# Performance work log

Measured on AMD Instinct MI355X. Metric: run time of the kernel, lower is better.

## Reference

```python
import jax, jax.numpy as jnp
import numpy as np

B, S, D_MODEL, D_INT = 4, 2048, 1024, 512
ALPHA = 0.3


def setup_inputs() -> dict:
    key = jax.random.key(0)
    ks = jax.random.split(key, 8)
    scale = 1.0 / np.sqrt(D_MODEL)
    inp = {
        "z_real": jax.random.normal(ks[0], (B, S, D_MODEL), dtype=jnp.float32),
        "z_imag": jax.random.normal(ks[1], (B, S, D_MODEL), dtype=jnp.float32),
        "Wq_r": jax.random.normal(ks[2], (D_MODEL, D_INT), dtype=jnp.float32) * scale,
        "Wq_i": jax.random.normal(ks[3], (D_MODEL, D_INT), dtype=jnp.float32) * scale,
        "Wk_r": jax.random.normal(ks[4], (D_MODEL, D_INT), dtype=jnp.float32) * scale,
        "Wk_i": jax.random.normal(ks[5], (D_MODEL, D_INT), dtype=jnp.float32) * scale,
        "Wv_r": jax.random.normal(ks[6], (D_MODEL, D_INT), dtype=jnp.float32) * scale,
        "Wv_i": jax.random.normal(ks[7], (D_MODEL, D_INT), dtype=jnp.float32) * scale,
    }
    return inp


def _complex_proj(zr, zi, Wr, Wi):
    # (zr + i*zi) @ (Wr + i*Wi) computed via 4 real matmuls, as in the torch code
    out_r = zr @ Wr - zi @ Wi
    out_i = zi @ Wr + zr @ Wi
    return out_r + 1j * out_i  # complex64


def reference(z_real, z_imag, Wq_r, Wq_i, Wk_r, Wk_i, Wv_r, Wv_i):
    q = _complex_proj(z_real, z_imag, Wq_r, Wq_i)  # [B,S,D_INT] complex64
    k = _complex_proj(z_real, z_imag, Wk_r, Wk_i)
    v = _complex_proj(z_real, z_imag, Wv_r, Wv_i)

    # attn_scores = q @ k^H : [B,S,S] complex64
    attn_scores = jnp.einsum("bsd,btd->bst", q, jnp.conj(k))

    # variant == 'hybrid': (|scores| + alpha*cos(angle(scores))) / sqrt(d_k)
    mag = jnp.abs(attn_scores)
    phase = jnp.cos(jnp.angle(attn_scores))
    scores = (mag + ALPHA * phase) / np.sqrt(D_INT)

    attn_weights = jax.nn.softmax(scores, axis=-1)  # [B,S,S] float32
    output = jnp.einsum("bst,btd->bsd", attn_weights.astype(jnp.complex64), v)
    return output, attn_weights
```

## Files before the change

### kernel.cpp

```cpp
#include <hip/hip_runtime.h>
#include <hip/hip_bf16.h>

typedef unsigned short u16;
typedef u16   u16x4 __attribute__((ext_vector_type(4)));
typedef u16   u16x8 __attribute__((ext_vector_type(8)));
typedef short v8s   __attribute__((ext_vector_type(8)));
typedef float fx4   __attribute__((ext_vector_type(4)));

#define DEVINL __device__ __forceinline__

DEVINL u16 f2bf(float x){
    unsigned u = __float_as_uint(x);
    u = u + 0x7FFFu + ((u >> 16) & 1u);
    return (u16)(u >> 16);
}
DEVINL float bf2f(u16 h){ return __uint_as_float(((unsigned)h) << 16); }

DEVINL void gload16(const u16* g, u16* l){
    __builtin_amdgcn_global_load_lds(
        (const __attribute__((address_space(1))) void*)g,
        (__attribute__((address_space(3))) void*)l, 16, 0, 0);
}

__global__ void convZ_kernel(const float* __restrict__ zr, const float* __restrict__ zi,
                             u16* __restrict__ Zh, u16* __restrict__ Zl){
    int idx = blockIdx.x * blockDim.x + threadIdx.x;
    size_t i4 = (size_t)idx * 4;
    int m = (int)(i4 >> 11);
    int c = (int)(i4 & 2047);
    const float* src = (c < 1024) ? (zr + (size_t)m*1024 + c)
                                  : (zi + (size_t)m*1024 + (c - 1024));
    fx4 v = *(const fx4*)src;
    u16x4 h, l;
#pragma unroll
    for (int j = 0; j < 4; j++){
        u16 hh = f2bf(v[j]); h[j] = hh; l[j] = f2bf(v[j] - bf2f(hh));
    }
    *(u16x4*)(Zh + i4) = h;
    *(u16x4*)(Zl + i4) = l;
}

__global__ void convW_kernel(const float* __restrict__ Wq_r, const float* __restrict__ Wq_i,
                             const float* __restrict__ Wk_r, const float* __restrict__ Wk_i,
                             const float* __restrict__ Wv_r, const float* __restrict__ Wv_i,
                             u16* __restrict__ Wth, u16* __restrict__ Wtl){
    __shared__ float t[32][33];
    int k0 = blockIdx.x * 32;
    int c0 = blockIdx.y * 32;
    int blk = c0 >> 9;  int j0 = c0 & 511;
    int pair = blk >> 1, ri = blk & 1;
    int hh = k0 >> 10;  int ks0 = k0 & 1023;
    const float* Ws[6] = {Wq_r, Wq_i, Wk_r, Wk_i, Wv_r, Wv_i};
    const float* src; float sign = 1.f;
    if (ri == 0){ if (hh == 0) src = Ws[pair*2]; else { src = Ws[pair*2+1]; sign = -1.f; } }
    else        { src = (hh == 0) ? Ws[pair*2+1] : Ws[pair*2]; }
    int tx = threadIdx.x, ty = threadIdx.y;
    for (int yy = ty; yy < 32; yy += 8)
        t[yy][tx] = src[(size_t)(ks0 + yy)*512 + j0 + tx];
    __syncthreads();
    for (int yy = ty; yy < 32; yy += 8){
        float v = sign * t[tx][yy];
        u16 h2 = f2bf(v);
        size_t o = (size_t)(c0 + yy)*2048 + k0 + tx;
        Wth[o] = h2;
        Wtl[o] = f2bf(v - bf2f(h2));
    }
}

__global__ void vt_kernel(const u16* __restrict__ C, int colOff, u16* __restrict__ Vt){
    __shared__ u16 t[32][34];
    int t0 = blockIdx.x * 32; int d0 = blockIdx.y * 32; int b = blockIdx.z;
    int tx = threadIdx.x, ty = threadIdx.y;
    const u16* src = C + (size_t)b*2048*3072 + colOff;
    for (int yy = ty; yy < 32; yy += 8)
        t[yy][tx] = src[(size_t)(t0 + yy)*3072 + d0 + tx];
    __syncthreads();
    u16* dst = Vt + (size_t)b*512*2048;
    for (int yy = ty; yy < 32; yy += 8)
        dst[(size_t)(d0 + yy)*2048 + t0 + tx] = t[tx][yy];
}

__global__ __launch_bounds__(256)
void softmax_kernel(float* __restrict__ H, const float* __restrict__ SiP, u16* __restrict__ Wbf){
    int row = blockIdx.x;
    float* p = H + (size_t)row * 2048;
    const float* q = SiP + (size_t)row * 2048;
    int tid = threadIdx.x;
    fx4 v[2];
#pragma unroll
    for (int i = 0; i < 2; i++){
        fx4 sr = *(fx4*)(p + i*1024 + tid*4);
        fx4 si = *(const fx4*)(q + i*1024 + tid*4);
#pragma unroll
        for (int j = 0; j < 4; j++){
            float mag = sqrtf(sr[j]*sr[j] + si[j]*si[j]);
            float ph  = sr[j] / fmaxf(mag, 1e-30f);
            v[i][j] = (mag + 0.3f*ph) * 0.044194173824159216f;
        }
    }
    float m = -1e30f;
#pragma unroll
    for (int i = 0; i < 2; i++)
#pragma unroll
        for (int j = 0; j < 4; j++) m = fmaxf(m, v[i][j]);
    for (int k = 1; k < 64; k <<= 1) m = fmaxf(m, __shfl_xor(m, k));
    __shared__ float sm[4], ss[4];
    int w = tid >> 6, lane = tid & 63;
    if (lane == 0) sm[w] = m;
    __syncthreads();
    m = fmaxf(fmaxf(sm[0], sm[1]), fmaxf(sm[2], sm[3]));
    float s = 0.f;
#pragma unroll
    for (int i = 0; i < 2; i++)
#pragma unroll
        for (int j = 0; j < 4; j++){ v[i][j] = __expf(v[i][j] - m); s += v[i][j]; }
    for (int k = 1; k < 64; k <<= 1) s += __shfl_xor(s, k);
    if (lane == 0) ss[w] = s;
    __syncthreads();
    s = ss[0] + ss[1] + ss[2] + ss[3];
    float inv = 1.f / s;
    u16* wb = Wbf + (size_t)row * 2048;
#pragma unroll
    for (int i = 0; i < 2; i++){
        fx4 o; u16x4 ob;
#pragma unroll
        for (int j = 0; j < 4; j++){ o[j] = v[i][j] * inv; ob[j] = f2bf(o[j]); }
        *(fx4*)(p + i*1024 + tid*4) = o;
        *(u16x4*)(wb + i*1024 + tid*4) = ob;
    }
}

__global__ __launch_bounds__(256, 2)
void score2_kernel(const u16* __restrict__ Chi, const u16* __restrict__ Clo,
                   float* __restrict__ Sr, float* __restrict__ Si)
{
    __shared__ u16 smem[8 * 4096];
    int z = blockIdx.z;
    int tid = threadIdx.x, lane = tid & 63, w = tid >> 6;
    int wm = w & 1, wn = w >> 1;
    int frow = lane & 15, g = lane >> 4;

    int srow = w * 32 + (lane >> 2);
    int scol = (lane & 3) * 8;
    size_t qoff = ((size_t)z*2048 + blockIdx.y*128 + srow) * 3072 + scol;
    size_t koff = ((size_t)z*2048 + blockIdx.x*128 + srow) * 3072 + 1024 + scol;
    u16* L = smem;

    v8s sgn8;
#pragma unroll
    for (int j = 0; j < 8; j++) sgn8[j] = (short)0x8000;

    fx4 aR[4][4] = {}, aI[4][4] = {};

    for (int kt = 0; kt < 16; ++kt){
        int k0 = kt * 32;
#pragma unroll
        for (int c = 0; c < 2; c++){
            size_t q = qoff + (size_t)c * 49152 + k0;
            size_t k = koff + (size_t)c * 49152 + k0;
            u16* d = L + w * 1024 + c * 512;
            gload16(Chi + q,       d);
            gload16(Clo + q,       d + 4096);
            gload16(Chi + q + 512, d + 8192);
            gload16(Clo + q + 512, d + 12288);
            gload16(Chi + k,       d + 16384);
            gload16(Clo + k,       d + 20480);
            gload16(Chi + k + 512, d + 24576);
            gload16(Clo + k + 512, d + 28672);
        }
        __syncthreads();

        v8s ar_h[4], ar_l[4], ai_h[4], ai_l[4];
#pragma unroll
        for (int mi = 0; mi < 4; mi++){
            int off = (wm*64 + mi*16 + frow) * 32 + g * 8;
            ar_h[mi] = *(const v8s*)(L + off);
            ar_l[mi] = *(const v8s*)(L + 4096  + off);
            ai_h[mi] = *(const v8s*)(L + 8192  + off);
            ai_l[mi] = *(const v8s*)(L + 12288 + off);
        }
#pragma unroll
        for (int ni = 0; ni < 4; ni++){
            int off = (wn*64 + ni*16 + frow) * 32 + g * 8;
            v8s br_h = *(const v8s*)(L + 16384 + off);
            v8s br_l = *(const v8s*)(L + 20480 + off);
            v8s bi_h = *(const v8s*)(L + 24576 + off);
            v8s bi_l = *(const v8s*)(L + 28672 + off);
            v8s bn_h = bi_h ^ sgn8;
            v8s bn_l = bi_l ^ sgn8;
#pragma unroll
            for (int mi = 0; mi < 4; mi++){
                aR[mi][ni] = __builtin_amdgcn_mfma_f32_16x16x32_bf16(ar_h[mi], br_h, aR[mi][ni], 0, 0, 0);
                aR[mi][ni] = __builtin_amdgcn_mfma_f32_16x16x32_bf16(ar_h[mi], br_l, aR[mi][ni], 0, 0, 0);
                aR[mi][ni] = __builtin_amdgcn_mfma_f32_16x16x32_bf16(ar_l[mi], br_h, aR[mi][ni], 0, 0, 0);
                aR[mi][ni] = __builtin_amdgcn_mfma_f32_16x16x32_bf16(ai_h[mi], bi_h, aR[mi][ni], 0, 0, 0);
                aR[mi][ni] = __builtin_amdgcn_mfma_f32_16x16x32_bf16(ai_h[mi], bi_l, aR[mi][ni], 0, 0, 0);
                aR[mi][ni] = __builtin_amdgcn_mfma_f32_16x16x32_bf16(ai_l[mi], bi_h, aR[mi][ni], 0, 0, 0);
                aI[mi][ni] = __builtin_amdgcn_mfma_f32_16x16x32_bf16(ai_h[mi], br_h, aI[mi][ni], 0, 0, 0);
                aI[mi][ni] = __builtin_amdgcn_mfma_f32_16x16x32_bf16(ai_h[mi], br_l, aI[mi][ni], 0, 0, 0);
                aI[mi][ni] = __builtin_amdgcn_mfma_f32_16x16x32_bf16(ai_l[mi], br_h, aI[mi][ni], 0, 0, 0);
                aI[mi][ni] = __builtin_amdgcn_mfma_f32_16x16x32_bf16(ar_h[mi], bn_h, aI[mi][ni], 0, 0, 0);
                aI[mi][ni] = __builtin_amdgcn_mfma_f32_16x16x32_bf16(ar_h[mi], bn_l, aI[mi][ni], 0, 0, 0);
                aI[mi][ni] = __builtin_amdgcn_mfma_f32_16x16x32_bf16(ar_l[mi], bn_h, aI[mi][ni], 0, 0, 0);
            }
        }
        __syncthreads();
    }

    size_t cb = (size_t)z * 2048 * 2048;
    int gcol0 = blockIdx.x * 128 + wn * 64;
    int grow0 = blockIdx.y * 128 + wm * 64;
    int rgrp  = (lane >> 4) * 4;
#pragma unroll
    for (int mi = 0; mi < 4; mi++)
#pragma unroll
        for (int ni = 0; ni < 4; ni++){
            int col = gcol0 + ni*16 + frow;
#pragma unroll
            for (int r = 0; r < 4; r++){
                size_t o = cb + (size_t)(grow0 + mi*16 + rgrp + r) * 2048 + col;
                Sr[o] = aR[mi][ni][r];
                Si[o] = aI[mi][ni][r];
            }
        }
}

template<int SPLIT, int EPI>
__global__ __launch_bounds__(256, 2)
void gemm_bt(const u16* __restrict__ Ah, const u16* __restrict__ Al,
             long long aBatch, int lda,
             const u16* __restrict__ Bh, const u16* __restrict__ Bl,
             long long bBatch, int ldb,
             float* __restrict__ Cf, u16* __restrict__ Ch, u16* __restrict__ Cl,
             long long cBatch, int ldc, int ostride, int nk)
{
    constexpr int NT = SPLIT ? 4 : 2;
    __shared__ u16 smem[NT * 8192];

    int z = blockIdx.z;
    const u16* Ab  = Ah + (size_t)(aBatch * z) + (size_t)blockIdx.y * 128 * lda;
    const u16* Bb  = Bh + (size_t)(bBatch * z) + (size_t)blockIdx.x * 128 * ldb;

    int tid = threadIdx.x;
    int lane = tid & 63, w = tid >> 6;
    int wm = w & 1, wn = w >> 1;
    int frow = lane & 15, g = lane >> 4;

    int srow = w * 32 + (lane >> 3);
    int slog = (lane & 7) ^ (lane >> 3);
    const u16* pA  = Ab + (size_t)srow * lda + slog * 8;
    const u16* pB  = Bb + (size_t)srow * ldb + slog * 8;
    const u16* pAl = nullptr; const u16* pBl = nullptr;
    if constexpr (SPLIT){
        pAl = Al + (size_t)(aBatch * z) + (size_t)blockIdx.y * 128 * lda + (size_t)srow * lda + slog * 8;
        pBl = Bl + (size_t)(bBatch * z) + (size_t)blockIdx.x * 128 * ldb + (size_t)srow * ldb + slog * 8;
    }
    u16* ldsA  = smem + w * 2048;
    u16* ldsB  = smem + 8192 + w * 2048;
    u16* ldsAl = smem + 16384 + w * 2048;
    u16* ldsBl = smem + 24576 + w * 2048;

    fx4 acc[4][4] = {};

    for (int kt = 0; kt < nk; ++kt){
#pragma unroll
        for (int c = 0; c < 4; c++){
            size_t ga = (size_t)c * 8 * lda;
            size_t gb = (size_t)c * 8 * ldb;
            gload16(pA + ga, ldsA + c * 512);
            gload16(pB + gb, ldsB + c * 512);
            if constexpr (SPLIT){
                gload16(pAl + ga, ldsAl + c * 512);
                gload16(pBl + gb, ldsBl + c * 512);
            }
        }
        __syncthreads();

#pragma unroll
        for (int s = 0; s < 2; s++){
            int ko = ((g + 4*s) ^ (frow & 7)) * 8;
            v8s a_h[4], b_h[4];
#pragma unroll
            for (int mi = 0; mi < 4; mi++)
                a_h[mi] = *(const v8s*)(smem + (wm*64 + mi*16 + frow)*64 + ko);
#pragma unroll
            for (int ni = 0; ni < 4; ni++)
                b_h[ni] = *(const v8s*)(smem + 8192 + (wn*64 + ni*16 + frow)*64 + ko);
            if constexpr (SPLIT){
                v8s a_l[4], b_l[4];
#pragma unroll
                for (int mi = 0; mi < 4; mi++)
                    a_l[mi] = *(const v8s*)(smem + 16384 + (wm*64 + mi*16 + frow)*64 + ko);
#pragma unroll
                for (int ni = 0; ni < 4; ni++)
                    b_l[ni] = *(const v8s*)(smem + 24576 + (wn*64 + ni*16 + frow)*64 + ko);
#pragma unroll
                for (int mi = 0; mi < 4; mi++)
#pragma unroll
                    for (int ni = 0; ni < 4; ni++){
                        acc[mi][ni] = __builtin_amdgcn_mfma_f32_16x16x32_bf16(a_h[mi], b_h[ni], acc[mi][ni], 0, 0, 0);
                        acc[mi][ni] = __builtin_amdgcn_mfma_f32_16x16x32_bf16(a_h[mi], b_l[ni], acc[mi][ni], 0, 0, 0);
                        acc[mi][ni] = __builtin_amdgcn_mfma_f32_16x16x32_bf16(a_l[mi], b_h[ni], acc[mi][ni], 0, 0, 0);
                    }
            } else {
#pragma unroll
                for (int mi = 0; mi < 4; mi++)
#pragma unroll
                    for (int ni = 0; ni < 4; ni++)
                        acc[mi][ni] = __builtin_amdgcn_mfma_f32_16x16x32_bf16(a_h[mi], b_h[ni], acc[mi][ni], 0, 0, 0);
            }
        }
        __syncthreads();
        pA += 64; pB += 64;
        if constexpr (SPLIT){ pAl += 64; pBl += 64; }
    }

    int gcol0 = blockIdx.x * 128 + wn * 64;
    int grow0 = blockIdx.y * 128 + wm * 64;
    int rgrp  = (lane >> 4) * 4;
    if constexpr (EPI == 0){
        float* Cb = Cf + (size_t)(cBatch * z);
#pragma unroll
        for (int mi = 0; mi < 4; mi++)
#pragma unroll
            for (int ni = 0; ni < 4; ni++){
                int col = gcol0 + ni*16 + frow;
#pragma unroll
                for (int r = 0; r < 4; r++){
                    int row = grow0 + mi*16 + rgrp + r;
                    Cb[((size_t)row * ldc + col) * (size_t)ostride] = acc[mi][ni][r];
                }
            }
    } else {
        u16* Chb = Ch + (size_t)(cBatch * z);
        u16* Clb = Cl + (size_t)(cBatch * z);
#pragma unroll
        for (int mi = 0; mi < 4; mi++)
#pragma unroll
            for (int ni = 0; ni < 4; ni++){
                int col = gcol0 + ni*16 + frow;
#pragma unroll
                for (int r = 0; r < 4; r++){
                    int row = grow0 + mi*16 + rgrp + r;
                    float v = acc[mi][ni][r];
                    u16 hh = f2bf(v);
                    size_t o = (size_t)row * ldc + col;
                    Chb[o] = hh;
                    Clb[o] = f2bf(v - bf2f(hh));
                }
            }
    }
}

extern "C" void kernel_launch(void* const* d_in, const int* in_sizes, int n_in,
                              void* d_out, int out_size, void* d_ws, size_t ws_size,
                              hipStream_t stream)
{
    const float* zr   = (const float*)d_in[0];
    const float* zi   = (const float*)d_in[1];
    const float* Wq_r = (const float*)d_in[2];
    const float* Wq_i = (const float*)d_in[3];
    const float* Wk_r = (const float*)d_in[4];
    const float* Wk_i = (const float*)d_in[5];
    const float* Wv_r = (const float*)d_in[6];
    const float* Wv_i = (const float*)d_in[7];

    constexpr long long Bn = 4, S = 2048, DI = 512;
    char* ws = (char*)d_ws;
    u16* Chi = (u16*)ws;
    u16* Clo = Chi + 25165824;
    char* ws2 = ws + 134217728;
    u16* Zh  = (u16*)ws2;
    u16* Zl  = Zh + 16777216;
    u16* Wth = Zl + 16777216;
    u16* Wtl = Wth + 6291456;
    float* bufX = (float*)ws2;
    u16* Vt  = (u16*)(ws2 + 67108864);
    u16* Vti = Vt + 4194304;
    u16* Wbf = (u16*)ws;

    long long attn_elems = Bn * S * S;
    bool interleaved = ((long long)out_size - attn_elems) == 2LL * Bn * S * DI;
    float* outP = (float*)d_out;
    float* attn = outP + ((long long)out_size - attn_elems);

    dim3 b256(256);
    convZ_kernel<<<16384, b256, 0, stream>>>(zr, zi, Zh, Zl);
    convW_kernel<<<dim3(64, 96), dim3(32, 8), 0, stream>>>(Wq_r, Wq_i, Wk_r, Wk_i, Wv_r, Wv_i, Wth, Wtl);

    gemm_bt<1,1><<<dim3(24, 64, 1), b256, 0, stream>>>(
        Zh, Zl, 0, 2048,
        Wth, Wtl, 0, 2048,
        nullptr, Chi, Clo, 0, 3072, 1, 2048/64);

    score2_kernel<<<dim3(16, 16, 4), b256, 0, stream>>>(Chi, Clo, attn, bufX);

    vt_kernel<<<dim3(64, 16, 4), dim3(32, 8), 0, stream>>>(Chi, 2048, Vt);
    if (interleaved)
        vt_kernel<<<dim3(64, 16, 4), dim3(32, 8), 0, stream>>>(Chi, 2560, Vti);

    softmax_kernel<<<8192, b256, 0, stream>>>(attn, bufX, Wbf);

    if (!interleaved){
        gemm_bt<0,0><<<dim3(4, 16, 4), b256, 0, stream>>>(
            Wbf, nullptr, 2048LL*2048, 2048,
            Vt, nullptr, 512LL*2048, 2048,
            outP, nullptr, nullptr, 2048LL*512, 512, 1, 2048/64);
    } else {
        gemm_bt<0,0><<<dim3(4, 16, 4), b256, 0, stream>>>(
            Wbf, nullptr, 2048LL*2048, 2048,
            Vt, nullptr, 512LL*2048, 2048,
            outP, nullptr, nullptr, 2048LL*512*2, 512, 2, 2048/64);
        gemm_bt<0,0><<<dim3(4, 16, 4), b256, 0, stream>>>(
            Wbf, nullptr, 2048LL*2048, 2048,
            Vti, nullptr, 512LL*2048, 2048,
            outP + 1, nullptr, nullptr, 2048LL*512*2, 512, 2, 2048/64);
    }
    (void)in_sizes; (void)n_in; (void)ws_size;
}
```

Before: 672.0 us.

## Fuse hybrid score transform into score epilogue and project V in plain bf16

The magnitude/phase score transform moves into the score GEMM epilogue, so it writes one fp32 score matrix instead of separate real and imaginary matrices that softmax must reread. Softmax now only loads precomputed scores. The V projection is split out of the split-bf16 (hi/lo) projection GEMM and runs as a cheaper single-bf16 GEMM. This lowers V precision because its low-order correction term is dropped.

Measured after the change: 643.7 us. -4.2%, faster.

```diff
diff --git a/kernel.cpp b/kernel.cpp
--- a/kernel.cpp
+++ b/kernel.cpp
@@ -81,23 +81,13 @@
 }
 
 __global__ __launch_bounds__(256)
-void softmax_kernel(float* __restrict__ H, const float* __restrict__ SiP, u16* __restrict__ Wbf){
+void softmax_kernel(float* __restrict__ H, u16* __restrict__ Wbf){
     int row = blockIdx.x;
     float* p = H + (size_t)row * 2048;
-    const float* q = SiP + (size_t)row * 2048;
     int tid = threadIdx.x;
     fx4 v[2];
-#pragma unroll
-    for (int i = 0; i < 2; i++){
-        fx4 sr = *(fx4*)(p + i*1024 + tid*4);
-        fx4 si = *(const fx4*)(q + i*1024 + tid*4);
-#pragma unroll
-        for (int j = 0; j < 4; j++){
-            float mag = sqrtf(sr[j]*sr[j] + si[j]*si[j]);
-            float ph  = sr[j] / fmaxf(mag, 1e-30f);
-            v[i][j] = (mag + 0.3f*ph) * 0.044194173824159216f;
-        }
-    }
+    v[0] = *(fx4*)(p + tid*4);
+    v[1] = *(fx4*)(p + 1024 + tid*4);
     float m = -1e30f;
 #pragma unroll
     for (int i = 0; i < 2; i++)
@@ -132,7 +122,7 @@
 
 __global__ __launch_bounds__(256, 2)
 void score2_kernel(const u16* __restrict__ Chi, const u16* __restrict__ Clo,
-                   float* __restrict__ Sr, float* __restrict__ Si)
+                   float* __restrict__ Y)
 {
     __shared__ u16 smem[8 * 4096];
     int z = blockIdx.z;
@@ -219,8 +209,10 @@
 #pragma unroll
             for (int r = 0; r < 4; r++){
                 size_t o = cb + (size_t)(grow0 + mi*16 + rgrp + r) * 2048 + col;
-                Sr[o] = aR[mi][ni][r];
-                Si[o] = aI[mi][ni][r];
+                float re = aR[mi][ni][r], im = aI[mi][ni][r];
+                float mag = sqrtf(re*re + im*im);
+                float ph  = re / fmaxf(mag, 1e-30f);
+                Y[o] = (mag + 0.3f*ph) * 0.044194173824159216f;
             }
         }
 }
@@ -331,7 +323,7 @@
                     Cb[((size_t)row * ldc + col) * (size_t)ostride] = acc[mi][ni][r];
                 }
             }
-    } else {
+    } else if constexpr (EPI == 1){
         u16* Chb = Ch + (size_t)(cBatch * z);
         u16* Clb = Cl + (size_t)(cBatch * z);
 #pragma unroll
@@ -347,6 +339,19 @@
                     size_t o = (size_t)row * ldc + col;
                     Chb[o] = hh;
                     Clb[o] = f2bf(v - bf2f(hh));
+                }
+            }
+    } else {
+        u16* Chb = Ch + (size_t)(cBatch * z);
+#pragma unroll
+        for (int mi = 0; mi < 4; mi++)
+#pragma unroll
+            for (int ni = 0; ni < 4; ni++){
+                int col = gcol0 + ni*16 + frow;
+#pragma unroll
+                for (int r = 0; r < 4; r++){
+                    int row = grow0 + mi*16 + rgrp + r;
+                    Chb[(size_t)row * ldc + col] = f2bf(acc[mi][ni][r]);
                 }
             }
     }
@@ -374,7 +379,6 @@
     u16* Zl  = Zh + 16777216;
     u16* Wth = Zl + 16777216;
     u16* Wtl = Wth + 6291456;
-    float* bufX = (float*)ws2;
     u16* Vt  = (u16*)(ws2 + 67108864);
     u16* Vti = Vt + 4194304;
     u16* Wbf = (u16*)ws;
@@ -388,18 +392,28 @@
     convZ_kernel<<<16384, b256, 0, stream>>>(zr, zi, Zh, Zl);
     convW_kernel<<<dim3(64, 96), dim3(32, 8), 0, stream>>>(Wq_r, Wq_i, Wk_r, Wk_i, Wv_r, Wv_i, Wth, Wtl);
 
-    gemm_bt<1,1><<<dim3(24, 64, 1), b256, 0, stream>>>(
+    gemm_bt<1,1><<<dim3(16, 64, 1), b256, 0, stream>>>(
         Zh, Zl, 0, 2048,
         Wth, Wtl, 0, 2048,
         nullptr, Chi, Clo, 0, 3072, 1, 2048/64);
 
-    score2_kernel<<<dim3(16, 16, 4), b256, 0, stream>>>(Chi, Clo, attn, bufX);
+    gemm_bt<0,4><<<dim3(4, 64, 1), b256, 0, stream>>>(
+        Zh, nullptr, 0, 2048,
+        Wth + (size_t)2048*2048, nullptr, 0, 2048,
+        nullptr, Chi + 2048, nullptr, 0, 3072, 1, 2048/64);
+    if (interleaved)
+        gemm_bt<0,4><<<dim3(4, 64, 1), b256, 0, stream>>>(
+            Zh, nullptr, 0, 2048,
+            Wth + (size_t)2560*2048, nullptr, 0, 2048,
+            nullptr, Chi + 2560, nullptr, 0, 3072, 1, 2048/64);
+
+    score2_kernel<<<dim3(16, 16, 4), b256, 0, stream>>>(Chi, Clo, attn);
 
     vt_kernel<<<dim3(64, 16, 4), dim3(32, 8), 0, stream>>>(Chi, 2048, Vt);
     if (interleaved)
         vt_kernel<<<dim3(64, 16, 4), dim3(32, 8), 0, stream>>>(Chi, 2560, Vti);
 
-    softmax_kernel<<<8192, b256, 0, stream>>>(attn, bufX, Wbf);
+    softmax_kernel<<<8192, b256, 0, stream>>>(attn, Wbf);
 
     if (!interleaved){
         gemm_bt<0,0><<<dim3(4, 16, 4), b256, 0, stream>>>(
```
